# Kernel tuning notes

Measured on AMD Instinct MI355X. Metric: run time of the kernel, lower is better.

Reference implementation:

```python
import jax, jax.numpy as jnp
import numpy as np

N_TOKENS = 524288
N_FEATURES = 128
N_MODELS = 16
N_LAYERS = 2


def setup_inputs() -> dict:
    key = jax.random.key(0)
    kx, kw, kb = jax.random.split(key, 3)
    x = jax.random.normal(kx, (N_TOKENS, N_FEATURES), dtype=jnp.float32)
    # per-expert, per-layer Linear weights in torch layout [out, in]
    scale = 1.0 / np.sqrt(N_FEATURES)
    W = jax.random.normal(kw, (N_MODELS, N_LAYERS, N_FEATURES, N_FEATURES), dtype=jnp.float32) * scale
    b = jax.random.normal(kb, (N_MODELS, N_LAYERS, N_FEATURES), dtype=jnp.float32) * scale
    return {"x": x, "W": W, "b": b}


def reference(x, W, b):
    # x: [N, F]; W: [M, L, F_out, F_in]; b: [M, L, F_out]
    # slices = M equal contiguous partitions of the token dim; each slice runs
    # through its own Linear+ReLU stack and is scattered back (here: reshape).
    M, L, Fo, Fi = W.shape
    xs = x.reshape(M, -1, Fi)  # [M, N/M, F] gathered slices
    for l in range(L):  # small fixed depth loop
        xs = jax.nn.relu(jnp.einsum('mnf,mgf->mng', xs, W[:, l]) + b[:, l][:, None, :])
    return xs.reshape(x.shape[0], Fo)
```

## Files before the change

### kernel.cpp

```cpp
#include <hip/hip_runtime.h>


#define NF   128
#define NM   16
#define NTOK 524288
#define TPM  (NTOK / NM)
#define BM   64
#define WPAD 136

typedef __attribute__((ext_vector_type(8))) short bf16x8;
typedef __attribute__((ext_vector_type(4))) float f32x4;

__device__ __forceinline__ unsigned short f2bf(float f) {
    union { float f; unsigned u; } v; v.f = f;
    unsigned r = v.u + 0x7FFFu + ((v.u >> 16) & 1u);
    return (unsigned short)(r >> 16);
}

__global__ __launch_bounds__(256, 2) void mlp16_kernel(
        const float* __restrict__ x, const float* __restrict__ W,
        const float* __restrict__ b, float* __restrict__ out) {
    __shared__ alignas(16) unsigned short sW[NF * WPAD];
    __shared__ alignas(16) unsigned short sY[BM * WPAD];
    __shared__ float sB[2 * NF];

    const int t    = threadIdx.x;
    const int wave = t >> 6;
    const int lane = t & 63;
    const int ln   = lane & 15;
    const int q    = lane >> 4;

    const int m    = blockIdx.x >> 9;
    const int tile = blockIdx.x & 511;
    const int row0 = m * TPM + tile * BM;

    sB[t] = b[m * 2 * NF + t];

    const float4* W0 = (const float4*)(W + (size_t)m * 2 * NF * NF);
    #pragma unroll
    for (int i = 0; i < 16; ++i) {
        int c = t + i * 256;
        float4 w = W0[c];
        unsigned short* d = &sW[(c >> 5) * WPAD + (c & 31) * 4];
        d[0] = f2bf(w.x); d[1] = f2bf(w.y); d[2] = f2bf(w.z); d[3] = f2bf(w.w);
    }
    __syncthreads();

    f32x4 acc[8];
    #pragma unroll
    for (int gt = 0; gt < 8; ++gt) acc[gt] = (f32x4){0.f, 0.f, 0.f, 0.f};

    const float* xrow = x + (size_t)(row0 + wave * 16 + ln) * NF;
    #pragma unroll
    for (int kt = 0; kt < 4; ++kt) {
        const int f0 = kt * 32 + q * 8;
        float4 a0 = *(const float4*)(xrow + f0);
        float4 a1 = *(const float4*)(xrow + f0 + 4);
        bf16x8 af;
        af[0] = (short)f2bf(a0.x); af[1] = (short)f2bf(a0.y);
        af[2] = (short)f2bf(a0.z); af[3] = (short)f2bf(a0.w);
        af[4] = (short)f2bf(a1.x); af[5] = (short)f2bf(a1.y);
        af[6] = (short)f2bf(a1.z); af[7] = (short)f2bf(a1.w);
        #pragma unroll
        for (int gt = 0; gt < 8; ++gt) {
            bf16x8 bfr = *(const bf16x8*)&sW[(gt * 16 + ln) * WPAD + f0];
            acc[gt] = __builtin_amdgcn_mfma_f32_16x16x32_bf16(af, bfr, acc[gt], 0, 0, 0);
        }
    }

    #pragma unroll
    for (int gt = 0; gt < 8; ++gt) {
        const float bias = sB[gt * 16 + ln];
        #pragma unroll
        for (int r = 0; r < 4; ++r) {
            float v = acc[gt][r] + bias;
            v = v > 0.f ? v : 0.f;
            sY[(wave * 16 + q * 4 + r) * WPAD + gt * 16 + ln] = f2bf(v);
        }
    }
    __syncthreads();

    const float4* W1 = W0 + (NF * NF / 4);
    #pragma unroll
    for (int i = 0; i < 16; ++i) {
        int c = t + i * 256;
        float4 w = W1[c];
        unsigned short* d = &sW[(c >> 5) * WPAD + (c & 31) * 4];
        d[0] = f2bf(w.x); d[1] = f2bf(w.y); d[2] = f2bf(w.z); d[3] = f2bf(w.w);
    }
    __syncthreads();

    f32x4 acc2[8];
    #pragma unroll
    for (int gt = 0; gt < 8; ++gt) acc2[gt] = (f32x4){0.f, 0.f, 0.f, 0.f};

    const unsigned short* yrow = &sY[(wave * 16 + ln) * WPAD];
    #pragma unroll
    for (int kt = 0; kt < 4; ++kt) {
        const int f0 = kt * 32 + q * 8;
        bf16x8 af = *(const bf16x8*)(yrow + f0);
        #pragma unroll
        for (int gt = 0; gt < 8; ++gt) {
            bf16x8 bfr = *(const bf16x8*)&sW[(gt * 16 + ln) * WPAD + f0];
            acc2[gt] = __builtin_amdgcn_mfma_f32_16x16x32_bf16(af, bfr, acc2[gt], 0, 0, 0);
        }
    }

    #pragma unroll
    for (int gt = 0; gt < 8; ++gt) {
        const float bias = sB[NF + gt * 16 + ln];
        #pragma unroll
        for (int r = 0; r < 4; ++r) {
            float v = acc2[gt][r] + bias;
            v = v > 0.f ? v : 0.f;
            out[(size_t)(row0 + wave * 16 + q * 4 + r) * NF + gt * 16 + ln] = v;
        }
    }
}

extern "C" void kernel_launch(void* const* d_in, const int* in_sizes, int n_in,
                              void* d_out, int out_size, void* d_ws, size_t ws_size,
                              hipStream_t stream) {
    const float* x = (const float*)d_in[0];
    const float* W = (const float*)d_in[1];
    const float* b = (const float*)d_in[2];
    float* out = (float*)d_out;
    mlp16_kernel<<<dim3(NTOK / BM), dim3(256), 0, stream>>>(x, W, b, out);
}
```

Measured before the change: 469.7 us.

## Process four row tiles per block to amortize per-expert weight loading

Each block now handles four 64-row tiles instead of one, so the fp32-to-bf16 weight conversion into shared memory happens once per 256 rows rather than once per 64. Layer-1 results for all tiles are kept packed in registers until the second weight matrix is loaded, then staged through shared memory one tile at a time for layer 2. The occupancy hint rises from 2 to 3 blocks per CU. The cost is higher register pressure from the 64 packed values per thread, and a grid four times smaller.

Result: slower. 623.6 us (+32.8%).

```diff
diff --git a/kernel.cpp b/kernel.cpp
--- a/kernel.cpp
+++ b/kernel.cpp
@@ -6,6 +6,8 @@
 #define NTOK 524288
 #define TPM  (NTOK / NM)
 #define BM   64
+#define TILES 4
+#define BLK_PER_M (TPM / (BM * TILES))
 #define WPAD 136
 
 typedef __attribute__((ext_vector_type(8))) short bf16x8;
@@ -16,8 +18,11 @@
     unsigned r = v.u + 0x7FFFu + ((v.u >> 16) & 1u);
     return (unsigned short)(r >> 16);
 }
+__device__ __forceinline__ unsigned f2bf2(float lo, float hi) {
+    return (unsigned)f2bf(lo) | ((unsigned)f2bf(hi) << 16);
+}
 
-__global__ __launch_bounds__(256, 2) void mlp16_kernel(
+__global__ __launch_bounds__(256, 3) void mlp16_kernel(
         const float* __restrict__ x, const float* __restrict__ W,
         const float* __restrict__ b, float* __restrict__ out) {
     __shared__ alignas(16) unsigned short sW[NF * WPAD];
@@ -30,57 +35,61 @@
     const int ln   = lane & 15;
     const int q    = lane >> 4;
 
-    const int m    = blockIdx.x >> 9;
-    const int tile = blockIdx.x & 511;
-    const int row0 = m * TPM + tile * BM;
+    const int m   = blockIdx.x / BLK_PER_M;
+    const int blk = blockIdx.x % BLK_PER_M;
+    const size_t row0 = (size_t)m * TPM + (size_t)blk * (BM * TILES);
 
     sB[t] = b[m * 2 * NF + t];
 
-    const float4* W0 = (const float4*)(W + (size_t)m * 2 * NF * NF);
+    const float4* Wm = (const float4*)(W + (size_t)m * 2 * NF * NF);
     #pragma unroll
     for (int i = 0; i < 16; ++i) {
         int c = t + i * 256;
-        float4 w = W0[c];
+        float4 w = Wm[c];
         unsigned short* d = &sW[(c >> 5) * WPAD + (c & 31) * 4];
         d[0] = f2bf(w.x); d[1] = f2bf(w.y); d[2] = f2bf(w.z); d[3] = f2bf(w.w);
     }
     __syncthreads();
 
-    f32x4 acc[8];
+    unsigned ypk[TILES][16];
+
     #pragma unroll
-    for (int gt = 0; gt < 8; ++gt) acc[gt] = (f32x4){0.f, 0.f, 0.f, 0.f};
+    for (int tt = 0; tt < TILES; ++tt) {
+        f32x4 acc[8];
+        #pragma unroll
+        for (int g = 0; g < 8; ++g) acc[g] = (f32x4){0.f, 0.f, 0.f, 0.f};
 
-    const float* xrow = x + (size_t)(row0 + wave * 16 + ln) * NF;
-    #pragma unroll
-    for (int kt = 0; kt < 4; ++kt) {
-        const int f0 = kt * 32 + q * 8;
-        float4 a0 = *(const float4*)(xrow + f0);
-        float4 a1 = *(const float4*)(xrow + f0 + 4);
-        bf16x8 af;
-        af[0] = (short)f2bf(a0.x); af[1] = (short)f2bf(a0.y);
-        af[2] = (short)f2bf(a0.z); af[3] = (short)f2bf(a0.w);
-        af[4] = (short)f2bf(a1.x); af[5] = (short)f2bf(a1.y);
-        af[6] = (short)f2bf(a1.z); af[7] = (short)f2bf(a1.w);
+        const float* xrow = x + (row0 + tt * BM + wave * 16 + ln) * NF;
         #pragma unroll
-        for (int gt = 0; gt < 8; ++gt) {
-            bf16x8 bfr = *(const bf16x8*)&sW[(gt * 16 + ln) * WPAD + f0];
-            acc[gt] = __builtin_amdgcn_mfma_f32_16x16x32_bf16(af, bfr, acc[gt], 0, 0, 0);
+        for (int kt = 0; kt < 4; ++kt) {
+            const int f0 = kt * 32 + q * 8;
+            float4 a0 = *(const float4*)(xrow + f0);
+            float4 a1 = *(const float4*)(xrow + f0 + 4);
+            bf16x8 af;
+            af[0] = (short)f2bf(a0.x); af[1] = (short)f2bf(a0.y);
+            af[2] = (short)f2bf(a0.z); af[3] = (short)f2bf(a0.w);
+            af[4] = (short)f2bf(a1.x); af[5] = (short)f2bf(a1.y);
+            af[6] = (short)f2bf(a1.z); af[7] = (short)f2bf(a1.w);
+            #pragma unroll
+            for (int g = 0; g < 8; ++g) {
+                bf16x8 bfr = *(const bf16x8*)&sW[(g * 16 + ln) * WPAD + f0];
+                acc[g] = __builtin_amdgcn_mfma_f32_16x16x32_bf16(af, bfr, acc[g], 0, 0, 0);
+            }
+        }
+        #pragma unroll
+        for (int g = 0; g < 8; ++g) {
+            const float bias = sB[g * 16 + ln];
+            float v0 = fmaxf(acc[g][0] + bias, 0.f);
+            float v1 = fmaxf(acc[g][1] + bias, 0.f);
+            float v2 = fmaxf(acc[g][2] + bias, 0.f);
+            float v3 = fmaxf(acc[g][3] + bias, 0.f);
+            ypk[tt][g * 2]     = f2bf2(v0, v1);
+            ypk[tt][g * 2 + 1] = f2bf2(v2, v3);
         }
     }
 
-    #pragma unroll
-    for (int gt = 0; gt < 8; ++gt) {
-        const float bias = sB[gt * 16 + ln];
-        #pragma unroll
-        for (int r = 0; r < 4; ++r) {
-            float v = acc[gt][r] + bias;
-            v = v > 0.f ? v : 0.f;
-            sY[(wave * 16 + q * 4 + r) * WPAD + gt * 16 + ln] = f2bf(v);
-        }
-    }
     __syncthreads();
-
-    const float4* W1 = W0 + (NF * NF / 4);
+    const float4* W1 = Wm + (NF * NF / 4);
     #pragma unroll
     for (int i = 0; i < 16; ++i) {
         int c = t + i * 256;
@@ -90,30 +99,41 @@
     }
     __syncthreads();
 
-    f32x4 acc2[8];
     #pragma unroll
-    for (int gt = 0; gt < 8; ++gt) acc2[gt] = (f32x4){0.f, 0.f, 0.f, 0.f};
+    for (int tt = 0; tt < TILES; ++tt) {
+        #pragma unroll
+        for (int g = 0; g < 8; ++g) {
+            #pragma unroll
+            for (int p = 0; p < 2; ++p) {
+                unsigned d = ypk[tt][g * 2 + p];
+                sY[(wave * 16 + q * 4 + 2 * p)     * WPAD + g * 16 + ln] = (unsigned short)(d & 0xFFFFu);
+                sY[(wave * 16 + q * 4 + 2 * p + 1) * WPAD + g * 16 + ln] = (unsigned short)(d >> 16);
+            }
+        }
+        f32x4 acc[8];
+        #pragma unroll
+        for (int g = 0; g < 8; ++g) acc[g] = (f32x4){0.f, 0.f, 0.f, 0.f};
 
-    const unsigned short* yrow = &sY[(wave * 16 + ln) * WPAD];
-    #pragma unroll
-    for (int kt = 0; kt < 4; ++kt) {
-        const int f0 = kt * 32 + q * 8;
-        bf16x8 af = *(const bf16x8*)(yrow + f0);
+        const unsigned short* yrow = &sY[(wave * 16 + ln) * WPAD];
         #pragma unroll
-        for (int gt = 0; gt < 8; ++gt) {
-            bf16x8 bfr = *(const bf16x8*)&sW[(gt * 16 + ln) * WPAD + f0];
-            acc2[gt] = __builtin_amdgcn_mfma_f32_16x16x32_bf16(af, bfr, acc2[gt], 0, 0, 0);
+        for (int kt = 0; kt < 4; ++kt) {
+            const int f0 = kt * 32 + q * 8;
+            bf16x8 af = *(const bf16x8*)(yrow + f0);
+            #pragma unroll
+            for (int g = 0; g < 8; ++g) {
+                bf16x8 bfr = *(const bf16x8*)&sW[(g * 16 + ln) * WPAD + f0];
+                acc[g] = __builtin_amdgcn_mfma_f32_16x16x32_bf16(af, bfr, acc[g], 0, 0, 0);
+            }
         }
-    }
-
-    #pragma unroll
-    for (int gt = 0; gt < 8; ++gt) {
-        const float bias = sB[NF + gt * 16 + ln];
+        float* orow = out + (row0 + tt * BM + wave * 16) * NF;
         #pragma unroll
-        for (int r = 0; r < 4; ++r) {
-            float v = acc2[gt][r] + bias;
-            v = v > 0.f ? v : 0.f;
-            out[(size_t)(row0 + wave * 16 + q * 4 + r) * NF + gt * 16 + ln] = v;
+        for (int g = 0; g < 8; ++g) {
+            const float bias = sB[NF + g * 16 + ln];
+            #pragma unroll
+            for (int r = 0; r < 4; ++r) {
+                float v = fmaxf(acc[g][r] + bias, 0.f);
+                orow[(size_t)(q * 4 + r) * NF + g * 16 + ln] = v;
+            }
         }
     }
 }
@@ -125,5 +145,5 @@
     const float* W = (const float*)d_in[1];
     const float* b = (const float*)d_in[2];
     float* out = (float*)d_out;
-    mlp16_kernel<<<dim3(NTOK / BM), dim3(256), 0, stream>>>(x, W, b, out);
+    mlp16_kernel<<<dim3(NM * BLK_PER_M), dim3(256), 0, stream>>>(x, W, b, out);
 }
```
